# Kernel tuning notes

Measured on AMD Instinct MI355X. Metric: run time of the kernel, lower is better.

Reference implementation:

```python
import jax, jax.numpy as jnp
import numpy as np

N, L, F, C, H, D = 2, 512, 128, 64, 12, 16
INF = 1e5
SQ29 = float(np.sqrt(2.0 / 9.0))
SCALE = float(np.sqrt(1.0 / 3.0))
EPS_DIR = 1e-4
LN_EPS = 1e-5


def setup_inputs() -> dict:
    key = jax.random.key(0)
    ks = jax.random.split(key, 16)
    s = 0.02
    return {
        "R": jax.random.normal(ks[0], (N, L, 3, 3), jnp.float32),
        "t": jax.random.normal(ks[1], (N, L, 3), jnp.float32),
        "p_CB": jax.random.normal(ks[2], (N, L, 3), jnp.float32),
        "x": jax.random.normal(ks[3], (N, L, F), jnp.float32),
        "z": jax.random.normal(ks[4], (N, L, L, C), jnp.float32),
        "mask": jax.random.randint(ks[5], (N, L), 0, 2).astype(bool),
        "Wq": jax.random.normal(ks[6], (H * D, F), jnp.float32) * s,
        "Wk": jax.random.normal(ks[7], (H * D, F), jnp.float32) * s,
        "Wv": jax.random.normal(ks[8], (H * D, F), jnp.float32) * s,
        "Wpb": jax.random.normal(ks[9], (H, C), jnp.float32) * s,
        "gamma_raw": jnp.full((1, 1, 1, H), float(np.log(np.e - 1.0)), jnp.float32),
        "Wout": jax.random.normal(ks[10], (F, H * C + H * D + H * 7), jnp.float32) * s,
        "bout": jnp.zeros((F,), jnp.float32),
        "ln_w": jnp.ones((F,), jnp.float32),
        "ln_b": jnp.zeros((F,), jnp.float32),
    }


def reference(R, t, p_CB, x, z, mask, Wq, Wk, Wv, Wpb, gamma_raw, Wout, bout, ln_w, ln_b):
    # --- logits ---
    q = (x @ Wq.T).reshape(N, L, H, D)  # (N,L,H,D)
    k = (x @ Wk.T).reshape(N, L, H, D)
    v = (x @ Wv.T).reshape(N, L, H, D)
    logits_node = jnp.einsum('nihd,njhd->nijh', q, k)
    logits_pair = jnp.einsum('nijc,hc->nijh', z, Wpb)
    # CB squared distances, identical for all heads -> broadcast over H
    d2 = jnp.sum((p_CB[:, :, None, :] - p_CB[:, None, :, :]) ** 2, axis=-1)[..., None]  # (N,L,L,1)
    gamma = jax.nn.softplus(gamma_raw)  # (1,1,1,H)
    logits_beta = d2 * (-gamma * SQ29 / 2.0)
    logits = (logits_node + logits_pair + logits_beta) * SCALE
    # --- masked softmax over axis j (2) ---
    mask_row = mask[:, :, None, None]
    mask_pair = mask_row & mask[:, None, :, None]
    logits = jnp.where(mask_pair, logits, logits - INF)
    alpha = jax.nn.softmax(logits, axis=2)
    alpha = jnp.where(mask_row, alpha, jnp.zeros_like(alpha))  # (N,L,L,H)
    # --- pair aggregation ---
    feat_p2n = jnp.einsum('nijh,nijc->nihc', alpha, z).reshape(N, L, H * C)
    # --- node aggregation ---
    feat_node = jnp.einsum('nijh,njhd->nihd', alpha, v).reshape(N, L, H * D)
    # --- beta (CB point) aggregation ---
    aggr = jnp.einsum('nijh,njc->nihc', alpha, p_CB)  # (N,L,H,3) in global frame
    local = jnp.einsum('nlji,nlhj->nlhi', R, aggr - t[:, :, None, :])  # global_to_local: R^T (q - t)
    dist = jnp.linalg.norm(local, axis=-1)  # (N,L,H)
    direction = local / (dist[..., None] + EPS_DIR)
    feat_spatial = jnp.concatenate(
        [local.reshape(N, L, -1), dist.reshape(N, L, -1), direction.reshape(N, L, -1)], axis=-1)
    # --- output transform + residual layernorm ---
    feat_all = jnp.concatenate([feat_p2n, feat_node, feat_spatial], axis=-1) @ Wout.T + bout
    feat_all = jnp.where(mask[:, :, None], feat_all, 0.0)
    y = x + feat_all
    mu = jnp.mean(y, axis=-1, keepdims=True)
    var = jnp.var(y, axis=-1, keepdims=True)
    return (y - mu) / jnp.sqrt(var + LN_EPS) * ln_w + ln_b
```

## Files before the change

### kernel.cpp

```cpp
#include <hip/hip_runtime.h>
#include <hip/hip_bf16.h>

constexpr int NB   = 2;
constexpr int LL   = 512;
constexpr int LLP  = 516;
constexpr int FF   = 128;
constexpr int CC   = 64;
constexpr int HH   = 12;
constexpr int DD   = 16;
constexpr int HD   = HH * DD;
constexpr int FEAT = HH*CC + HH*DD + HH*7;
constexpr float INFV   = 100000.0f;
constexpr float SCALEF = 0.57735026918962576f;
constexpr float SQ29H  = 0.23570226039551584f;

__global__ void compact_kernel(const int* __restrict__ maskg, int* __restrict__ row_map)
{
    const int tid = threadIdx.x;
    const int lane = tid & 63, wv = tid >> 6;
    __shared__ int s_cnt[16];
    __shared__ int s_off[16];
    __shared__ int s_tot;
    const int m = maskg[tid] ? 1 : 0;
    unsigned long long b = __ballot(m);
    const int pre = __popcll(b & ((1ull << lane) - 1ull));
    if (lane == 0) s_cnt[wv] = __popcll(b);
    __syncthreads();
    if (tid == 0) {
        int s = 0;
        for (int w = 0; w < 16; ++w) { s_off[w] = s; s += s_cnt[w]; }
        s_tot = s;
    }
    __syncthreads();
    const int nact = s_off[wv] + pre;
    if (m) row_map[nact] = tid;
    else   row_map[s_tot + (tid - nact)] = tid;
}

__global__ __launch_bounds__(192) void qkv_kernel(
    const float* __restrict__ xg, const float* __restrict__ Wq,
    const float* __restrict__ Wk, const float* __restrict__ Wv,
    float* __restrict__ q_ws, float* __restrict__ kT4, float* __restrict__ vT)
{
    const int b = blockIdx.x;
    const int t = threadIdx.x;
    __shared__ __align__(16) float sx[4*FF];
    __shared__ __align__(16) float sw[3*HD*20];

    for (int o = t; o < 4*FF; o += 192) sx[o] = xg[(size_t)b*4*FF + o];

    float aq[4] = {0.f,0.f,0.f,0.f};
    float ak[4] = {0.f,0.f,0.f,0.f};
    float av[4] = {0.f,0.f,0.f,0.f};

    for (int ft = 0; ft < 8; ++ft) {
        __syncthreads();
        #pragma unroll
        for (int m = 0; m < 3; ++m) {
            const float* W = (m == 0) ? Wq : ((m == 1) ? Wk : Wv);
            #pragma unroll
            for (int p = 0; p < 4; ++p) {
                const int r = (t >> 2) + 48*p, q = t & 3;
                float4 v = *(const float4*)(W + (size_t)r*FF + ft*16 + q*4);
                *(float4*)&sw[m*3840 + r*20 + q*4] = v;
            }
        }
        __syncthreads();
        const float* wq = &sw[0*3840 + t*20];
        const float* wk = &sw[1*3840 + t*20];
        const float* wv = &sw[2*3840 + t*20];
        #pragma unroll
        for (int f4 = 0; f4 < 4; ++f4) {
            float4 a  = *(const float4*)&wq[f4*4];
            float4 bq = *(const float4*)&wk[f4*4];
            float4 cq = *(const float4*)&wv[f4*4];
            #pragma unroll
            for (int r = 0; r < 4; ++r) {
                float4 xv = *(const float4*)&sx[r*FF + ft*16 + f4*4];
                aq[r] += xv.x*a.x  + xv.y*a.y  + xv.z*a.z  + xv.w*a.w;
                ak[r] += xv.x*bq.x + xv.y*bq.y + xv.z*bq.z + xv.w*bq.w;
                av[r] += xv.x*cq.x + xv.y*cq.y + xv.z*cq.z + xv.w*cq.w;
            }
        }
    }
    const int n = (b*4) >> 9, i0 = (b*4) & 511;
    #pragma unroll
    for (int r = 0; r < 4; ++r) {
        const int row = b*4 + r, i = i0 + r;
        q_ws[(size_t)row*HD + t] = aq[r];
        kT4[(((size_t)n*48 + (t >> 2))*LL + i)*4 + (t & 3)] = ak[r];
    }
    *(float4*)&vT[((size_t)n*HD + t)*LL + i0] = make_float4(av[0], av[1], av[2], av[3]);
}

__global__ __launch_bounds__(512, 2) void attn_kernel(
    const float* __restrict__ Rg, const float* __restrict__ tg, const float* __restrict__ pg,
    const float* __restrict__ xg, const float* __restrict__ zg, const int* __restrict__ maskg,
    const float* __restrict__ Wpbg, const float* __restrict__ gammag,
    const float* __restrict__ Woutg, const float* __restrict__ boutg,
    const float* __restrict__ lnwg, const float* __restrict__ lnbg,
    const float* __restrict__ q_ws, const float* __restrict__ kT4, const float* __restrict__ vT,
    const int* __restrict__ row_map, float* __restrict__ outg)
{
    const int row = row_map[blockIdx.x];
    const int n = row >> 9;
    const int tid = threadIdx.x;

    __shared__ __align__(16) float s_exp[HH*LLP];
    __shared__ __align__(16) float s_big[4*768];
    __shared__ __align__(16) float s_p[3*LL];
    __shared__ __align__(16) float s_q[HD];
    __shared__ __align__(16) float s_x[FF];
    __shared__ __align__(16) float s_y[FF];
    __shared__ __align__(16) float s_f[FEAT];
    __shared__ float s_aggr[36];
    __shared__ float s_inv[HH];
    __shared__ float s_coef[HH];
    __shared__ float s_geo[15];
    __shared__ float s_red[2];

    if (tid < FF) s_x[tid] = xg[(size_t)row*FF + tid];
    if (tid >= 128 && tid < 128 + HD) s_q[tid-128] = q_ws[(size_t)row*HD + (tid-128)];
    for (int o = tid; o < 3*LL; o += 512) s_p[o] = pg[(size_t)n*3*LL + o];
    if (tid >= 320 && tid < 332) {
        float g = gammag[tid-320];
        float gamma = log1pf(__expf(fminf(g, 80.0f)));
        s_coef[tid-320] = -gamma * SQ29H;
    }
    if (tid >= 332 && tid < 335) s_geo[tid-332] = pg[(size_t)row*3 + (tid-332)];
    if (tid >= 335 && tid < 338) s_geo[3 + tid-335] = tg[(size_t)row*3 + (tid-335)];
    if (tid >= 338 && tid < 347) s_geo[6 + tid-338] = Rg[(size_t)row*9 + (tid-338)];
    const int mi = maskg[row];
    __syncthreads();

    if (mi) {
        {
            const int j = tid;
            float acc[HH];

            const float* zr = zg + ((size_t)row*LL + j)*CC;
            float4 zv[16];
            #pragma unroll
            for (int c4 = 0; c4 < 16; ++c4) zv[c4] = ((const float4*)zr)[c4];
            #pragma unroll
            for (int h = 0; h < HH; ++h) {
                const float4* wh = (const float4*)(Wpbg + h*CC);
                float a = 0.f;
                #pragma unroll
                for (int c4 = 0; c4 < 16; ++c4) {
                    float4 w = wh[c4];
                    a += zv[c4].x*w.x + zv[c4].y*w.y + zv[c4].z*w.z + zv[c4].w*w.w;
                }
                acc[h] = a;
            }
            const float* kb = kT4 + ((size_t)(n*48)*LL + j)*4;
            #pragma unroll
            for (int g = 0; g < 6; ++g) {
                float4 kv[8];
                #pragma unroll
                for (int u = 0; u < 8; ++u)
                    kv[u] = *(const float4*)(kb + (size_t)(g*8+u)*LL*4);
                #pragma unroll
                for (int u = 0; u < 8; ++u) {
                    const int hd4 = g*8+u;
                    float4 q4v = *(const float4*)&s_q[hd4*4];
                    acc[hd4 >> 2] += q4v.x*kv[u].x + q4v.y*kv[u].y + q4v.z*kv[u].z + q4v.w*kv[u].w;
                }
            }
            float e0 = s_geo[0]-s_p[j*3+0];
            float e1 = s_geo[1]-s_p[j*3+1];
            float e2 = s_geo[2]-s_p[j*3+2];
            float d2 = e0*e0 + e1*e1 + e2*e2;
            const float sub = maskg[n*LL + j] ? 0.0f : INFV;
            #pragma unroll
            for (int h = 0; h < HH; ++h) {
                float lg = (acc[h] + d2*s_coef[h]) * SCALEF - sub;
                s_exp[h*LLP + j] = __expf(fminf(lg, 80.0f));
            }
        }
        __syncthreads();

        {
            const int wv = tid >> 6, lane = tid & 63;
            if (wv < 4) {
                const int c = lane, q4v = wv;
                float acc[HH];
                #pragma unroll
                for (int h = 0; h < HH; ++h) acc[h] = 0.f;
                const float* zb = zg + ((size_t)row*LL + q4v*128)*CC + c;
                const float* ep = s_exp + q4v*128;
                #pragma unroll 2
                for (int jj = 0; jj < 128; jj += 8) {
                    float z0 = zb[(size_t)(jj+0)*CC];
                    float z1 = zb[(size_t)(jj+1)*CC];
                    float z2 = zb[(size_t)(jj+2)*CC];
                    float z3 = zb[(size_t)(jj+3)*CC];
                    float z4 = zb[(size_t)(jj+4)*CC];
                    float z5 = zb[(size_t)(jj+5)*CC];
                    float z6 = zb[(size_t)(jj+6)*CC];
                    float z7 = zb[(size_t)(jj+7)*CC];
                    #pragma unroll
                    for (int h = 0; h < HH; ++h) {
                        float4 ea = *(const float4*)&ep[h*LLP + jj];
                        float4 eb = *(const float4*)&ep[h*LLP + jj + 4];
                        acc[h] += ea.x*z0 + ea.y*z1 + ea.z*z2 + ea.w*z3
                                + eb.x*z4 + eb.y*z5 + eb.z*z6 + eb.w*z7;
                    }
                }
                #pragma unroll
                for (int h = 0; h < HH; ++h) s_big[q4v*768 + h*64 + c] = acc[h];
            } else if (tid < 448) {
                const int w = (tid >> 6) - 4;
                const int hsub = lane >> 4;
                const int jj = lane & 15;
                const int wbase = w * 64;
                #pragma unroll 2
                for (int g = 0; g < 16; ++g) {
                    const int hd = wbase + g*4 + hsub;
                    const float* vb = vT + ((size_t)n*HD + hd)*LL;
                    const float* ep = s_exp + (hd >> 4)*LLP;
                    float a = 0.f;
                    #pragma unroll
                    for (int t8 = 0; t8 < 8; ++t8) {
                        float4 vv = *(const float4*)(vb + (jj + 16*t8)*4);
                        float4 ev = *(const float4*)(ep + (jj + 16*t8)*4);
                        a += vv.x*ev.x + vv.y*ev.y + vv.z*ev.z + vv.w*ev.w;
                    }
                    a += __shfl_xor(a, 1, 64);
                    a += __shfl_xor(a, 2, 64);
                    a += __shfl_xor(a, 4, 64);
                    a += __shfl_xor(a, 8, 64);
                    if (jj == 0) s_f[768 + hd] = a;
                }
            } else {
                const int o = tid - 448;
                for (int h = 0; h < HH; ++h) {
                    float s = 0.f;
                    #pragma unroll
                    for (int r = 0; r < 8; ++r) s += s_exp[h*LLP + lane + (r<<6)];
                    #pragma unroll
                    for (int off = 32; off > 0; off >>= 1) s += __shfl_xor(s, off, 64);
                    if (lane == 0) s_inv[h] = 1.0f / fmaxf(s, 1e-30f);
                }
                if (o < 36) {
                    const int h = o / 3, ax = o - h*3;
                    const float* ep = s_exp + h*LLP;
                    float a = 0.f;
                    #pragma unroll 8
                    for (int j = 0; j < LL; ++j) a += ep[j] * s_p[j*3 + ax];
                    s_aggr[o] = a;
                }
            }
        }
        __syncthreads();

        for (int o = tid; o < 960; o += 512) {
            if (o < 768)
                s_f[o] = (s_big[o] + s_big[768+o] + s_big[1536+o] + s_big[2304+o]) * s_inv[o >> 6];
            else
                s_f[o] = s_f[o] * s_inv[(o - 768) >> 4];
        }
        if (tid >= 500) {
            const int h = tid - 500;
            const float iv = s_inv[h];
            float m0 = s_aggr[h*3+0]*iv - s_geo[3];
            float m1 = s_aggr[h*3+1]*iv - s_geo[4];
            float m2 = s_aggr[h*3+2]*iv - s_geo[5];
            const float* Rm = &s_geo[6];
            float l0 = Rm[0]*m0 + Rm[3]*m1 + Rm[6]*m2;
            float l1 = Rm[1]*m0 + Rm[4]*m1 + Rm[7]*m2;
            float l2 = Rm[2]*m0 + Rm[5]*m1 + Rm[8]*m2;
            float dist = sqrtf(l0*l0 + l1*l1 + l2*l2);
            float idn = 1.0f/(dist + 1e-4f);
            s_f[960 + h*3+0] = l0; s_f[960 + h*3+1] = l1; s_f[960 + h*3+2] = l2;
            s_f[996 + h] = dist;
            s_f[1008 + h*3+0] = l0*idn; s_f[1008 + h*3+1] = l1*idn; s_f[1008 + h*3+2] = l2*idn;
        }
        __syncthreads();

        {
            const int f = tid >> 2, q4 = tid & 3;
            const float* wr = Woutg + (size_t)f * FEAT;
            float acc = 0.f;
            #pragma unroll 4
            for (int kk = q4*4; kk < FEAT; kk += 16) {
                float4 fv  = *(const float4*)&s_f[kk];
                float4 wvv = *(const float4*)(wr + kk);
                acc += fv.x*wvv.x + fv.y*wvv.y + fv.z*wvv.z + fv.w*wvv.w;
            }
            acc += __shfl_xor(acc, 1, 64);
            acc += __shfl_xor(acc, 2, 64);
            if (q4 == 0) s_y[f] = s_x[f] + boutg[f] + acc;
        }
    } else {
        if (tid < FF) s_y[tid] = s_x[tid];
    }
    __syncthreads();

    if (tid < 64) {
        float a = s_y[tid], b = s_y[tid + 64];
        float s1 = a + b, s2 = a*a + b*b;
        #pragma unroll
        for (int off = 32; off > 0; off >>= 1) {
            s1 += __shfl_xor(s1, off, 64);
            s2 += __shfl_xor(s2, off, 64);
        }
        if (tid == 0) { s_red[0] = s1; s_red[1] = s2; }
    }
    __syncthreads();
    if (tid < FF) {
        float mu  = s_red[0] * (1.0f/FF);
        float var = s_red[1] * (1.0f/FF) - mu*mu;
        float vv = (s_y[tid] - mu) * rsqrtf(fmaxf(var, 0.0f) + 1e-5f);
        vv = vv * lnwg[tid] + lnbg[tid];
        outg[(size_t)row*FF + tid] = vv;
    }
}

extern "C" void kernel_launch(void* const* d_in, const int* in_sizes, int n_in,
                              void* d_out, int out_size, void* d_ws, size_t ws_size,
                              hipStream_t stream) {
    const float* Rg    = (const float*)d_in[0];
    const float* tg    = (const float*)d_in[1];
    const float* pg    = (const float*)d_in[2];
    const float* xg    = (const float*)d_in[3];
    const float* zg    = (const float*)d_in[4];
    const int*   maskg = (const int*)d_in[5];
    const float* Wq    = (const float*)d_in[6];
    const float* Wk    = (const float*)d_in[7];
    const float* Wv    = (const float*)d_in[8];
    const float* Wpb   = (const float*)d_in[9];
    const float* gam   = (const float*)d_in[10];
    const float* Wout  = (const float*)d_in[11];
    const float* bout  = (const float*)d_in[12];
    const float* lnw   = (const float*)d_in[13];
    const float* lnb   = (const float*)d_in[14];
    float* outp = (float*)d_out;

    float* q_ws = (float*)d_ws;
    float* kT4  = q_ws + (size_t)NB*LL*HD;
    float* vT   = kT4  + (size_t)NB*LL*HD;
    int*   row_map = (int*)(vT + (size_t)NB*LL*HD);

    compact_kernel<<<1, NB*LL, 0, stream>>>(maskg, row_map);
    qkv_kernel<<<NB*LL/4, HD, 0, stream>>>(xg, Wq, Wk, Wv, q_ws, kT4, vT);
    attn_kernel<<<NB*LL, 512, 0, stream>>>(Rg, tg, pg, xg, zg, maskg,
                                           Wpb, gam, Wout, bout, lnw, lnb,
                                           q_ws, kT4, vT, row_map, outp);
}
```

Before: 263.0 us.

## Restructure per-row attention reductions for coalesced loads and register reuse

Reads q straight from global memory instead of staging it in shared memory, and widens the z-row unroll in the pair aggregation from 8 to 16 rows per step. The node aggregation, normalizer and CB-point aggregation are reorganized so each lane handles a contiguous 8-element slice of j, followed by full-wavefront shuffle reductions. The normalizer and point aggregation are merged into a single pass. The output projection now keeps the feature vector in registers and gives each wave 16 output rows with coalesced Wout loads. These changes aim to cut LDS traffic, serial loops and uncoalesced accesses, at the cost of more shuffles and higher register pressure.

New measurement: 346.1 us. 1.32x slower.

```diff
diff --git a/kernel.cpp b/kernel.cpp
--- a/kernel.cpp
+++ b/kernel.cpp
@@ -109,10 +109,9 @@
     __shared__ __align__(16) float s_exp[HH*LLP];
     __shared__ __align__(16) float s_big[4*768];
     __shared__ __align__(16) float s_p[3*LL];
-    __shared__ __align__(16) float s_q[HD];
     __shared__ __align__(16) float s_x[FF];
     __shared__ __align__(16) float s_y[FF];
-    __shared__ __align__(16) float s_f[FEAT];
+    __shared__ __align__(16) float s_f[1280];
     __shared__ float s_aggr[36];
     __shared__ float s_inv[HH];
     __shared__ float s_coef[HH];
@@ -120,7 +119,7 @@
     __shared__ float s_red[2];
 
     if (tid < FF) s_x[tid] = xg[(size_t)row*FF + tid];
-    if (tid >= 128 && tid < 128 + HD) s_q[tid-128] = q_ws[(size_t)row*HD + (tid-128)];
+    if (tid < 236) s_f[1044 + tid] = 0.f;
     for (int o = tid; o < 3*LL; o += 512) s_p[o] = pg[(size_t)n*3*LL + o];
     if (tid >= 320 && tid < 332) {
         float g = gammag[tid-320];
@@ -153,6 +152,7 @@
                 }
                 acc[h] = a;
             }
+            const float* qp = q_ws + (size_t)row*HD;
             const float* kb = kT4 + ((size_t)(n*48)*LL + j)*4;
             #pragma unroll
             for (int g = 0; g < 6; ++g) {
@@ -163,7 +163,7 @@
                 #pragma unroll
                 for (int u = 0; u < 8; ++u) {
                     const int hd4 = g*8+u;
-                    float4 q4v = *(const float4*)&s_q[hd4*4];
+                    float4 q4v = *(const float4*)(qp + hd4*4);
                     acc[hd4 >> 2] += q4v.x*kv[u].x + q4v.y*kv[u].y + q4v.z*kv[u].z + q4v.w*kv[u].w;
                 }
             }
@@ -189,66 +189,70 @@
                 for (int h = 0; h < HH; ++h) acc[h] = 0.f;
                 const float* zb = zg + ((size_t)row*LL + q4v*128)*CC + c;
                 const float* ep = s_exp + q4v*128;
-                #pragma unroll 2
-                for (int jj = 0; jj < 128; jj += 8) {
-                    float z0 = zb[(size_t)(jj+0)*CC];
-                    float z1 = zb[(size_t)(jj+1)*CC];
-                    float z2 = zb[(size_t)(jj+2)*CC];
-                    float z3 = zb[(size_t)(jj+3)*CC];
-                    float z4 = zb[(size_t)(jj+4)*CC];
-                    float z5 = zb[(size_t)(jj+5)*CC];
-                    float z6 = zb[(size_t)(jj+6)*CC];
-                    float z7 = zb[(size_t)(jj+7)*CC];
+                for (int jj = 0; jj < 128; jj += 16) {
+                    float zr16[16];
+                    #pragma unroll
+                    for (int u = 0; u < 16; ++u) zr16[u] = zb[(size_t)(jj+u)*CC];
                     #pragma unroll
                     for (int h = 0; h < HH; ++h) {
-                        float4 ea = *(const float4*)&ep[h*LLP + jj];
-                        float4 eb = *(const float4*)&ep[h*LLP + jj + 4];
-                        acc[h] += ea.x*z0 + ea.y*z1 + ea.z*z2 + ea.w*z3
-                                + eb.x*z4 + eb.y*z5 + eb.z*z6 + eb.w*z7;
+                        float4 e0 = *(const float4*)&ep[h*LLP + jj];
+                        float4 e1 = *(const float4*)&ep[h*LLP + jj + 4];
+                        float4 e2 = *(const float4*)&ep[h*LLP + jj + 8];
+                        float4 e3 = *(const float4*)&ep[h*LLP + jj + 12];
+                        acc[h] += e0.x*zr16[0] + e0.y*zr16[1] + e0.z*zr16[2] + e0.w*zr16[3]
+                                + e1.x*zr16[4] + e1.y*zr16[5] + e1.z*zr16[6] + e1.w*zr16[7]
+                                + e2.x*zr16[8] + e2.y*zr16[9] + e2.z*zr16[10]+ e2.w*zr16[11]
+                                + e3.x*zr16[12]+ e3.y*zr16[13]+ e3.z*zr16[14]+ e3.w*zr16[15];
                     }
                 }
                 #pragma unroll
                 for (int h = 0; h < HH; ++h) s_big[q4v*768 + h*64 + c] = acc[h];
             } else if (tid < 448) {
-                const int w = (tid >> 6) - 4;
-                const int hsub = lane >> 4;
-                const int jj = lane & 15;
-                const int wbase = w * 64;
-                #pragma unroll 2
-                for (int g = 0; g < 16; ++g) {
-                    const int hd = wbase + g*4 + hsub;
-                    const float* vb = vT + ((size_t)n*HD + hd)*LL;
-                    const float* ep = s_exp + (hd >> 4)*LLP;
-                    float a = 0.f;
+                const int w = wv - 4;
+                for (int hh = 0; hh < 4; ++hh) {
+                    const int h = w*4 + hh;
+                    const float* ep = s_exp + h*LLP + lane*8;
+                    float4 ea = *(const float4*)ep;
+                    float4 eb = *(const float4*)(ep + 4);
+                    const float* vb = vT + ((size_t)n*HD + h*16)*LL + lane*8;
+                    for (int d = 0; d < 16; ++d) {
+                        const float* vp = vb + (size_t)d*LL;
+                        float4 va = *(const float4*)vp;
+                        float4 v2 = *(const float4*)(vp + 4);
+                        float a = ea.x*va.x + ea.y*va.y + ea.z*va.z + ea.w*va.w
+                                + eb.x*v2.x + eb.y*v2.y + eb.z*v2.z + eb.w*v2.w;
+                        #pragma unroll
+                        for (int off = 32; off > 0; off >>= 1) a += __shfl_xor(a, off, 64);
+                        if (lane == 0) s_f[768 + h*16 + d] = a;
+                    }
+                }
+            } else {
+                float pp[24];
+                #pragma unroll
+                for (int u = 0; u < 6; ++u)
+                    *(float4*)&pp[u*4] = *(const float4*)&s_p[lane*24 + u*4];
+                for (int h = 0; h < HH; ++h) {
+                    const float* ep = s_exp + h*LLP + lane*8;
+                    float4 ea = *(const float4*)ep;
+                    float4 eb = *(const float4*)(ep + 4);
+                    float s  = ea.x+ea.y+ea.z+ea.w + eb.x+eb.y+eb.z+eb.w;
+                    float a0 = ea.x*pp[0] + ea.y*pp[3] + ea.z*pp[6]  + ea.w*pp[9]
+                             + eb.x*pp[12]+ eb.y*pp[15]+ eb.z*pp[18] + eb.w*pp[21];
+                    float a1 = ea.x*pp[1] + ea.y*pp[4] + ea.z*pp[7]  + ea.w*pp[10]
+                             + eb.x*pp[13]+ eb.y*pp[16]+ eb.z*pp[19] + eb.w*pp[22];
+                    float a2 = ea.x*pp[2] + ea.y*pp[5] + ea.z*pp[8]  + ea.w*pp[11]
+                             + eb.x*pp[14]+ eb.y*pp[17]+ eb.z*pp[20] + eb.w*pp[23];
                     #pragma unroll
-                    for (int t8 = 0; t8 < 8; ++t8) {
-                        float4 vv = *(const float4*)(vb + (jj + 16*t8)*4);
-                        float4 ev = *(const float4*)(ep + (jj + 16*t8)*4);
-                        a += vv.x*ev.x + vv.y*ev.y + vv.z*ev.z + vv.w*ev.w;
-                    }
-                    a += __shfl_xor(a, 1, 64);
-                    a += __shfl_xor(a, 2, 64);
-                    a += __shfl_xor(a, 4, 64);
-                    a += __shfl_xor(a, 8, 64);
-                    if (jj == 0) s_f[768 + hd] = a;
-                }
-            } else {
-                const int o = tid - 448;
-                for (int h = 0; h < HH; ++h) {
-                    float s = 0.f;
-                    #pragma unroll
-                    for (int r = 0; r < 8; ++r) s += s_exp[h*LLP + lane + (r<<6)];
-                    #pragma unroll
-                    for (int off = 32; off > 0; off >>= 1) s += __shfl_xor(s, off, 64);
-                    if (lane == 0) s_inv[h] = 1.0f / fmaxf(s, 1e-30f);
-                }
-                if (o < 36) {
-                    const int h = o / 3, ax = o - h*3;
-                    const float* ep = s_exp + h*LLP;
-                    float a = 0.f;
-                    #pragma unroll 8
-                    for (int j = 0; j < LL; ++j) a += ep[j] * s_p[j*3 + ax];
-                    s_aggr[o] = a;
+                    for (int off = 32; off > 0; off >>= 1) {
+                        s  += __shfl_xor(s,  off, 64);
+                        a0 += __shfl_xor(a0, off, 64);
+                        a1 += __shfl_xor(a1, off, 64);
+                        a2 += __shfl_xor(a2, off, 64);
+                    }
+                    if (lane == 0) {
+                        s_inv[h] = 1.0f / fmaxf(s, 1e-30f);
+                        s_aggr[h*3+0] = a0; s_aggr[h*3+1] = a1; s_aggr[h*3+2] = a2;
+                    }
                 }
             }
         }
@@ -279,18 +283,27 @@
         __syncthreads();
 
         {
-            const int f = tid >> 2, q4 = tid & 3;
-            const float* wr = Woutg + (size_t)f * FEAT;
-            float acc = 0.f;
-            #pragma unroll 4
-            for (int kk = q4*4; kk < FEAT; kk += 16) {
-                float4 fv  = *(const float4*)&s_f[kk];
-                float4 wvv = *(const float4*)(wr + kk);
-                acc += fv.x*wvv.x + fv.y*wvv.y + fv.z*wvv.z + fv.w*wvv.w;
-            }
-            acc += __shfl_xor(acc, 1, 64);
-            acc += __shfl_xor(acc, 2, 64);
-            if (q4 == 0) s_y[f] = s_x[f] + boutg[f] + acc;
+            const int wv = tid >> 6, lane = tid & 63;
+            float4 sf[5];
+            #pragma unroll
+            for (int u = 0; u < 5; ++u) sf[u] = *(const float4*)&s_f[(lane + 64*u)*4];
+            const int f0 = wv*16;
+            for (int fi = 0; fi < 16; ++fi) {
+                const int f = f0 + fi;
+                const float* wr = Woutg + (size_t)f * FEAT;
+                float acc = 0.f;
+                #pragma unroll
+                for (int u = 0; u < 5; ++u) {
+                    const int k4 = lane + 64*u;
+                    if (k4 < 261) {
+                        float4 w4 = *(const float4*)(wr + k4*4);
+                        acc += sf[u].x*w4.x + sf[u].y*w4.y + sf[u].z*w4.z + sf[u].w*w4.w;
+                    }
+                }
+                #pragma unroll
+                for (int off = 32; off > 0; off >>= 1) acc += __shfl_xor(acc, off, 64);
+                if (lane == 0) s_y[f] = s_x[f] + boutg[f] + acc;
+            }
         }
     } else {
         if (tid < FF) s_y[tid] = s_x[tid];
```
